# Performance work log

Measured on AMD Instinct MI355X. Metric: run time of the kernel, lower is better.

The kernel has to match this reference:

```python
import jax, jax.numpy as jnp
import numpy as np

B, N, D_IN, D_OUT = 8, 256, 128, 128


def setup_inputs() -> dict:
    key = jax.random.key(0)
    k1, k2, k3, k4, k5 = jax.random.split(key, 5)
    hidden = jax.random.normal(k1, (B, N, D_IN), dtype=jnp.float32)
    adj = jax.random.uniform(k2, (B, N, N), dtype=jnp.float32)
    dep_embed = jax.random.normal(k3, (B, N, N, D_IN), dtype=jnp.float32)
    weight = jax.random.normal(k4, (D_IN, D_OUT), dtype=jnp.float32) * 0.05
    bias_weight = jax.random.normal(k5, (D_OUT,), dtype=jnp.float32) * 0.05
    return {"hidden": hidden, "adj": adj, "dep_embed": dep_embed,
            "weight": weight, "bias_weight": bias_weight}


def reference(hidden, adj, dep_embed, weight, bias_weight):
    # fusion[b,p,q,d] = (hidden[b,p] + dep_embed[b,p,q]) @ W   (broadcast instead of tile)
    fusion = jnp.einsum('bpqe,ed->bpqd', hidden[:, :, None, :] + dep_embed, weight)
    # out[b,i,d] = sum_j adj[b,i,j] * fusion[b,j,i,d]   (transpose+mask+reduce fused)
    out = jnp.einsum('bij,bjid->bid', adj, fusion)
    return out + bias_weight
```

## Files before the change

### kernel.cpp

```cpp
#include <hip/hip_runtime.h>


constexpr int Bc = 8;
constexpr int Nc = 256;
constexpr int Dc = 128;
constexpr int JC  = 8;
constexpr int NCH = Nc / JC;
constexpr int ISP = 4;
constexpr int IW  = Nc / ISP;

typedef float floatx4 __attribute__((ext_vector_type(4)));

__global__ __launch_bounds__(256) void depgcn_pass1(
    const float* __restrict__ hidden,
    const float* __restrict__ adj,
    const float* __restrict__ dep,
    float* __restrict__ U)
{
    const int blk = blockIdx.x;
    const int ih  = blk & (ISP - 1);
    const int jc  = (blk >> 2) & (NCH - 1);
    const int b   = blk >> 7;
    const int t   = threadIdx.x;

    const int i0 = ih * IW;
    const int j0 = jc * JC;

    __shared__ float sA[JC][IW];
    {
        const int idx = t * 2;
        const int il  = idx >> 3;
        const int jl  = idx & 7;
        const float* ap = adj + ((size_t)b * Nc + i0 + il) * Nc + j0 + jl;
        sA[jl][il]     = ap[0];
        sA[jl + 1][il] = ap[1];
    }
    __syncthreads();

    floatx4 acc[8];
    #pragma unroll
    for (int k = 0; k < 8; ++k) acc[k] = {0.f, 0.f, 0.f, 0.f};

    const int e4 = (t & 31) * 4;
    const int r0 = t >> 5;

    const float* depBase = dep + (((size_t)(b * Nc + j0)) * Nc + i0) * Dc + t * 4;
    const float* hidBase = hidden + ((size_t)(b * Nc + j0)) * Dc + e4;

    for (int jl = 0; jl < JC; ++jl) {
        const float* dp = depBase + (size_t)jl * Nc * Dc;
        floatx4 d[8];
        #pragma unroll
        for (int k = 0; k < 8; ++k)
            d[k] = *(const floatx4*)(dp + k * 1024);
        const floatx4 h = *(const floatx4*)(hidBase + (size_t)jl * Dc);
        #pragma unroll
        for (int k = 0; k < 8; ++k) {
            const float a = sA[jl][r0 + k * 8];
            acc[k] += a * (d[k] + h);
        }
    }

    float* up = U + (((size_t)jc * Bc + b) * ISP + ih) * (IW * Dc) + t * 4;
    #pragma unroll
    for (int k = 0; k < 8; ++k)
        *(floatx4*)(up + k * 1024) = acc[k];
}

__global__ __launch_bounds__(128) void depgcn_pass2(
    const float* __restrict__ U,
    const float* __restrict__ W,
    const float* __restrict__ bias,
    float* __restrict__ out)
{
    const int bi = blockIdx.x;
    const int b  = bi >> 8;
    const int i  = bi & (Nc - 1);
    const int ih = i >> 6;
    const int il = i & (IW - 1);
    const int t  = threadIdx.x;

    __shared__ float sT[Dc];

    float s = 0.f;
    const float* up = U + ((size_t)b * ISP + ih) * (IW * Dc) + (size_t)il * Dc + t;
    #pragma unroll
    for (int jc = 0; jc < NCH; ++jc)
        s += up[(size_t)jc * (Bc * ISP * IW * Dc)];
    sT[t] = s;
    __syncthreads();

    float o = 0.f;
    const float* wp = W + t;
    #pragma unroll 16
    for (int e = 0; e < Dc; ++e)
        o = fmaf(sT[e], wp[(size_t)e * Dc], o);
    out[((size_t)b * Nc + i) * Dc + t] = o + bias[t];
}

extern "C" void kernel_launch(void* const* d_in, const int* in_sizes, int n_in,
                              void* d_out, int out_size, void* d_ws, size_t ws_size,
                              hipStream_t stream) {
    const float* hidden = (const float*)d_in[0];
    const float* adj    = (const float*)d_in[1];
    const float* dep    = (const float*)d_in[2];
    const float* W      = (const float*)d_in[3];
    const float* bias   = (const float*)d_in[4];
    float* out          = (float*)d_out;
    float* U            = (float*)d_ws;

    depgcn_pass1<<<dim3(Bc * NCH * ISP), dim3(256), 0, stream>>>(hidden, adj, dep, U);
    depgcn_pass2<<<dim3(Bc * Nc), dim3(128), 0, stream>>>(U, W, bias, out);
}
```

Before: 386.8 us.

## Fuse adjacency reduction and weight projection into single kernel over full j range

Replaces the two-pass scheme, which wrote per-j-chunk partial sums to a workspace, with one kernel per 8-row i tile. That kernel reduces over all j and then applies the weight matrix and bias in shared memory. This removes the intermediate workspace write and read and the second launch, and uses nontemporal loads for the streamed dep tensor. In exchange the grid shrinks to 256 blocks with a long serial j loop, which risks lower memory-level parallelism.

Measured after the change: 347.1 us. 10.3% less time.

```diff
diff --git a/kernel.cpp b/kernel.cpp
--- a/kernel.cpp
+++ b/kernel.cpp
@@ -4,98 +4,90 @@
 constexpr int Bc = 8;
 constexpr int Nc = 256;
 constexpr int Dc = 128;
-constexpr int JC  = 8;
-constexpr int NCH = Nc / JC;
-constexpr int ISP = 4;
-constexpr int IW  = Nc / ISP;
+constexpr int IW = 8;
+constexpr int NB = Nc / IW;
 
 typedef float floatx4 __attribute__((ext_vector_type(4)));
 
-__global__ __launch_bounds__(256) void depgcn_pass1(
+__global__ __launch_bounds__(256) void depgcn_fused(
     const float* __restrict__ hidden,
     const float* __restrict__ adj,
     const float* __restrict__ dep,
-    float* __restrict__ U)
-{
-    const int blk = blockIdx.x;
-    const int ih  = blk & (ISP - 1);
-    const int jc  = (blk >> 2) & (NCH - 1);
-    const int b   = blk >> 7;
-    const int t   = threadIdx.x;
-
-    const int i0 = ih * IW;
-    const int j0 = jc * JC;
-
-    __shared__ float sA[JC][IW];
-    {
-        const int idx = t * 2;
-        const int il  = idx >> 3;
-        const int jl  = idx & 7;
-        const float* ap = adj + ((size_t)b * Nc + i0 + il) * Nc + j0 + jl;
-        sA[jl][il]     = ap[0];
-        sA[jl + 1][il] = ap[1];
-    }
-    __syncthreads();
-
-    floatx4 acc[8];
-    #pragma unroll
-    for (int k = 0; k < 8; ++k) acc[k] = {0.f, 0.f, 0.f, 0.f};
-
-    const int e4 = (t & 31) * 4;
-    const int r0 = t >> 5;
-
-    const float* depBase = dep + (((size_t)(b * Nc + j0)) * Nc + i0) * Dc + t * 4;
-    const float* hidBase = hidden + ((size_t)(b * Nc + j0)) * Dc + e4;
-
-    for (int jl = 0; jl < JC; ++jl) {
-        const float* dp = depBase + (size_t)jl * Nc * Dc;
-        floatx4 d[8];
-        #pragma unroll
-        for (int k = 0; k < 8; ++k)
-            d[k] = *(const floatx4*)(dp + k * 1024);
-        const floatx4 h = *(const floatx4*)(hidBase + (size_t)jl * Dc);
-        #pragma unroll
-        for (int k = 0; k < 8; ++k) {
-            const float a = sA[jl][r0 + k * 8];
-            acc[k] += a * (d[k] + h);
-        }
-    }
-
-    float* up = U + (((size_t)jc * Bc + b) * ISP + ih) * (IW * Dc) + t * 4;
-    #pragma unroll
-    for (int k = 0; k < 8; ++k)
-        *(floatx4*)(up + k * 1024) = acc[k];
-}
-
-__global__ __launch_bounds__(128) void depgcn_pass2(
-    const float* __restrict__ U,
     const float* __restrict__ W,
     const float* __restrict__ bias,
     float* __restrict__ out)
 {
-    const int bi = blockIdx.x;
-    const int b  = bi >> 8;
-    const int i  = bi & (Nc - 1);
-    const int ih = i >> 6;
-    const int il = i & (IW - 1);
-    const int t  = threadIdx.x;
+    const int blk = blockIdx.x;
+    const int ih  = blk & (NB - 1);
+    const int b   = blk >> 5;
+    const int t   = threadIdx.x;
+    const int i0  = ih * IW;
 
-    __shared__ float sT[Dc];
+    const int il = t >> 5;
+    const int e4 = (t & 31) * 4;
 
-    float s = 0.f;
-    const float* up = U + ((size_t)b * ISP + ih) * (IW * Dc) + (size_t)il * Dc + t;
-    #pragma unroll
-    for (int jc = 0; jc < NCH; ++jc)
-        s += up[(size_t)jc * (Bc * ISP * IW * Dc)];
-    sT[t] = s;
+    __shared__ float sA[IW][Nc];
+    __shared__ float sT[IW][Dc];
+
+    {
+        const float* ap = adj + ((size_t)b * Nc + i0) * Nc;
+        #pragma unroll
+        for (int k = 0; k < 8; ++k)
+            ((float*)sA)[t + k * 256] = ap[t + k * 256];
+    }
     __syncthreads();
 
-    float o = 0.f;
-    const float* wp = W + t;
-    #pragma unroll 16
-    for (int e = 0; e < Dc; ++e)
-        o = fmaf(sT[e], wp[(size_t)e * Dc], o);
-    out[((size_t)b * Nc + i) * Dc + t] = o + bias[t];
+    const float* depP = dep + (((size_t)b * Nc) * Nc + i0) * Dc + t * 4;
+    const float* hidP = hidden + (size_t)b * Nc * Dc + e4;
+
+    floatx4 acc = {0.f, 0.f, 0.f, 0.f};
+
+    for (int j0 = 0; j0 < Nc; j0 += 8) {
+        floatx4 d[8];
+        #pragma unroll
+        for (int k = 0; k < 8; ++k)
+            d[k] = __builtin_nontemporal_load(
+                (const floatx4*)(depP + (size_t)(j0 + k) * Nc * Dc));
+        #pragma unroll
+        for (int k = 0; k < 8; ++k) {
+            const floatx4 h = *(const floatx4*)(hidP + (size_t)(j0 + k) * Dc);
+            const float   a = sA[il][j0 + k];
+            acc += a * (d[k] + h);
+        }
+    }
+
+    *(floatx4*)&sT[il][e4] = acc;
+    __syncthreads();
+
+    __shared__ float sO[2][IW][Dc];
+    {
+        const int d = t & (Dc - 1);
+        const int h = t >> 7;
+        const float* wp = W + (size_t)(h * 64) * Dc + d;
+        float o[IW];
+        #pragma unroll
+        for (int r = 0; r < IW; ++r) o[r] = 0.f;
+        for (int e = 0; e < 64; ++e) {
+            const float w = wp[(size_t)e * Dc];
+            #pragma unroll
+            for (int r = 0; r < IW; ++r)
+                o[r] = fmaf(sT[r][h * 64 + e], w, o[r]);
+        }
+        #pragma unroll
+        for (int r = 0; r < IW; ++r) sO[h][r][d] = o[r];
+    }
+    __syncthreads();
+
+    {
+        float* op = out + ((size_t)b * Nc + i0) * Dc;
+        #pragma unroll
+        for (int k = 0; k < 4; ++k) {
+            const int idx = t + k * 256;
+            const int r   = idx >> 7;
+            const int d   = idx & (Dc - 1);
+            op[idx] = sO[0][r][d] + sO[1][r][d] + bias[d];
+        }
+    }
 }
 
 extern "C" void kernel_launch(void* const* d_in, const int* in_sizes, int n_in,
@@ -107,8 +99,6 @@
     const float* W      = (const float*)d_in[3];
     const float* bias   = (const float*)d_in[4];
     float* out          = (float*)d_out;
-    float* U            = (float*)d_ws;
 
-    depgcn_pass1<<<dim3(Bc * NCH * ISP), dim3(256), 0, stream>>>(hidden, adj, dep, U);
-    depgcn_pass2<<<dim3(Bc * Nc), dim3(128), 0, stream>>>(U, W, bias, out);
+    depgcn_fused<<<dim3(Bc * NB), dim3(256), 0, stream>>>(hidden, adj, dep, W, bias, out);
 }
```
